# Kernel optimization log

Measured on AMD Instinct MI355X. Metric: run time of the kernel, lower is better.

## Reference

```python
import jax, jax.numpy as jnp
import numpy as np

D = 1024      # input_dim == memory_dim
HID = 1024    # hid_dim
NEG = 1e30


def setup_inputs() -> dict:
    key = jax.random.key(0)
    ks = jax.random.split(key, 9)
    N, LD, LM = 8, 2048, 512
    s = 1.0 / np.sqrt(D)
    return {
        "input": jax.random.normal(ks[0], (N, LD, D), jnp.float32),
        "memory": jax.random.normal(ks[1], (N, LM, D), jnp.float32),
        "mask": jnp.ones((N, LM), jnp.float32),
        # input_linear_1 / memory_linear_1: Linear(d, 1, bias=False)
        "in1_w": jax.random.normal(ks[2], (D,), jnp.float32) * s,
        "mem1_w": jax.random.normal(ks[3], (D,), jnp.float32) * s,
        # input_linear_2 / memory_linear_2: Linear(d, hid, bias=True), stored [d, hid]
        "in2_w": jax.random.normal(ks[4], (D, HID), jnp.float32) * s,
        "in2_b": jax.random.normal(ks[5], (HID,), jnp.float32) * s,
        "mem2_w": jax.random.normal(ks[6], (D, HID), jnp.float32) * s,
        "mem2_b": jax.random.normal(ks[7], (HID,), jnp.float32) * s,
    }


def reference(input, memory, mask, in1_w, mem1_w, in2_w, in2_b, mem2_w, mem2_b):
    # dropout=0.0 / eval mode -> identity
    dot_scale = jnp.asarray(np.sqrt(D), input.dtype)
    input_dot = jnp.einsum("nld,d->nl", input, in1_w)[:, :, None]      # [N,Ld,1]
    memory_dot = jnp.einsum("nmd,d->nm", memory, mem1_w)[:, None, :]   # [N,1,Lm]
    cross_dot = jnp.einsum("nld,nmd->nlm", input, memory) / dot_scale  # [N,Ld,Lm]
    att = input_dot + memory_dot + cross_dot
    att = att - NEG * (1.0 - mask[:, None, :])

    inp2 = jnp.einsum("nld,dh->nlh", input, in2_w) + in2_b    # [N,Ld,hid]
    mem2 = jnp.einsum("nmd,dh->nmh", memory, mem2_w) + mem2_b  # [N,Lm,hid]

    weight_one = jax.nn.softmax(att, axis=-1)                 # [N,Ld,Lm]
    output_one = jnp.einsum("nlm,nmh->nlh", weight_one, mem2)  # [N,Ld,hid]

    weight_two = jax.nn.softmax(jnp.max(att, axis=-1), axis=-1)  # [N,Ld]
    output_two = jnp.einsum("nl,nlh->nh", weight_two, inp2)[:, None, :]  # [N,1,hid]

    out = jnp.concatenate(
        [inp2, output_one, inp2 * output_one, output_two * output_one], axis=-1
    )  # [N,Ld,4*hid]
    return out, mem2
```

## Files before the change

kernel.cpp:

```cpp
#include <hip/hip_runtime.h>

typedef unsigned short u16;
typedef __attribute__((ext_vector_type(8))) short short8;
typedef __attribute__((ext_vector_type(4))) float f32x4;
typedef __attribute__((ext_vector_type(4))) unsigned short u16x4;

#define NSEQ 8
#define LD 2048
#define LM 512
#define DD 1024
#define HID 1024
#define M1 (NSEQ*LD)
#define M2 (NSEQ*LM)

#define GLOAD_LDS16(gp, lp) __builtin_amdgcn_global_load_lds( \
    (const __attribute__((address_space(1))) unsigned int*)(gp), \
    (__attribute__((address_space(3))) unsigned int*)(lp), 16, 0, 0)

__device__ __forceinline__ u16 f2bf(float f) {
    union { float f; unsigned int i; } v; v.f = f;
    unsigned int r = v.i + 0x7fffu + ((v.i >> 16) & 1u);
    return (u16)(r >> 16);
}
__device__ __forceinline__ float bf2f(u16 u) {
    union { unsigned int i; float f; } v; v.i = ((unsigned int)u) << 16; return v.f;
}

__global__ __launch_bounds__(256) void prep_all(
    const float* __restrict__ input, const float* __restrict__ memory,
    const float* __restrict__ in1_w, const float* __restrict__ mem1_w,
    const float* __restrict__ mask,
    const float* __restrict__ in2_w, const float* __restrict__ mem2_w,
    u16* __restrict__ input_bf16, u16* __restrict__ memory_bf16,
    u16* __restrict__ in2_wt, u16* __restrict__ mem2_wt,
    float* __restrict__ idot, float* __restrict__ mdotm) {
    __shared__ float tile[32][33];
    const int b = blockIdx.x, t = threadIdx.x;
    if (b < M1 + M2) {
        const float* src; const float* w; u16* dst;
        if (b < M1) { src = input + (size_t)b * DD; w = in1_w;
                      dst = input_bf16 + (size_t)b * DD; }
        else { const int rm = b - M1; src = memory + (size_t)rm * DD; w = mem1_w;
               dst = memory_bf16 + (size_t)rm * DD; }
        f32x4 v = *(const f32x4*)(src + t * 4);
        f32x4 wv = *(const f32x4*)(w + t * 4);
        u16x4 o;
        #pragma unroll
        for (int i = 0; i < 4; i++) o[i] = f2bf(v[i]);
        *(u16x4*)(dst + t * 4) = o;
        float s = v[0]*wv[0] + v[1]*wv[1] + v[2]*wv[2] + v[3]*wv[3];
        #pragma unroll
        for (int off = 32; off; off >>= 1) s += __shfl_down(s, off);
        if ((t & 63) == 0) tile[0][t >> 6] = s;
        __syncthreads();
        if (t == 0) {
            const float d = tile[0][0] + tile[0][1] + tile[0][2] + tile[0][3];
            if (b < M1) idot[b] = d;
            else { const int rm = b - M1;
                   mdotm[rm] = d - 1e30f * (1.0f - mask[rm]); }
        }
    } else {
        const int wb = b - (M1 + M2);
        const int z = wb >> 10;
        const int tid = wb & 1023;
        const int c0 = (tid & 31) * 32, r0 = (tid >> 5) * 32;
        const float* src = z ? mem2_w : in2_w;
        u16* dst = z ? mem2_wt : in2_wt;
        const int tx = t & 31, ty = t >> 5;
        #pragma unroll
        for (int yy = ty; yy < 32; yy += 8)
            tile[yy][tx] = src[(size_t)(r0 + yy) * DD + c0 + tx];
        __syncthreads();
        #pragma unroll
        for (int yy = ty; yy < 32; yy += 8)
            dst[(size_t)(c0 + yy) * DD + r0 + tx] = f2bf(tile[tx][yy]);
    }
}

template <int NT>
__global__ __launch_bounds__(512, 1) void gemm_mem2(
    const u16* __restrict__ A, const u16* __restrict__ B,
    float* __restrict__ out0, const float* __restrict__ bias,
    u16* __restrict__ mem2t) {
    constexpr int AI = 2, BM = 128;
    constexpr int BUFE = (BM + 128) * 64;
    __shared__ __align__(16) u16 lds[3 * BUFE];
    const int t = threadIdx.x;
    const int lane = t & 63, wave = t >> 6;
    const int wm = wave >> 2, wn = wave & 3;
    const int lr = lane & 15, kg = lane >> 4;
    const int bid = blockIdx.y * 8 + blockIdx.x;
    const int swz = (bid & 7) * gridDim.y + (bid >> 3);
    const int m0 = (swz >> 3) * BM, n0 = (swz & 7) * 128;

    const int srow = lane >> 3;
    const u16* gA[AI];
    const u16* gB[2];
    #pragma unroll
    for (int i = 0; i < AI; i++) {
        const int c = wave * AI + i;
        const int colb = ((lane & 7) * 16) ^ ((((c << 2) + (lane >> 4)) & 7) << 4);
        gA[i] = A + (size_t)(m0 + c * 8 + srow) * DD + (colb >> 1);
    }
    #pragma unroll
    for (int i = 0; i < 2; i++) {
        const int c = wave * 2 + i;
        const int colb = ((lane & 7) * 16) ^ ((((c << 2) + (lane >> 4)) & 7) << 4);
        gB[i] = B + (size_t)(n0 + c * 8 + srow) * DD + (colb >> 1);
    }
    int offA[2 * AI], offB[2];
    #pragma unroll
    for (int i = 0; i < 2 * AI; i++) {
        const int row = wm * (BM / 2) + i * 16 + lr;
        offA[i] = (row * 128 + kg * 16) ^ (((row >> 1) & 7) << 4);
    }
    #pragma unroll
    for (int j = 0; j < 2; j++) {
        const int row = wn * 32 + j * 16 + lr;
        offB[j] = (BM * 64 * 2 + row * 128 + kg * 16) ^ (((row >> 1) & 7) << 4);
    }

    f32x4 acc[2 * AI][2];
    #pragma unroll
    for (int i = 0; i < 2 * AI; i++)
        #pragma unroll
        for (int j = 0; j < 2; j++) acc[i][j] = (f32x4){0.f, 0.f, 0.f, 0.f};

    #define STAGE(tt, buf) do {                                             \
        u16* la_ = &lds[(buf) * BUFE];                                      \
        u16* lb_ = la_ + BM * 64;                                           \
        const int ko_ = (tt) * 64;                                          \
        _Pragma("unroll")                                                   \
        for (int i_ = 0; i_ < AI; i_++)                                     \
            GLOAD_LDS16(gA[i_] + ko_, la_ + (wave * AI + i_) * 512);        \
        _Pragma("unroll")                                                   \
        for (int i_ = 0; i_ < 2; i_++)                                      \
            GLOAD_LDS16(gB[i_] + ko_, lb_ + (wave * 2 + i_) * 512);         \
    } while (0)

    STAGE(0, 0);
    STAGE(1, 1);
    asm volatile("s_waitcnt vmcnt(4)" ::: "memory");
    __builtin_amdgcn_s_barrier();
    __builtin_amdgcn_sched_barrier(0);

    int cb = 0, sb = 2;
    for (int tt = 0; tt < NT; ++tt) {
        if (tt + 2 < NT) STAGE(tt + 2, sb);
        __builtin_amdgcn_sched_barrier(0);
        const char* bb = (const char*)&lds[cb * BUFE];
        short8 bfr[2][2];
        #pragma unroll
        for (int j = 0; j < 2; j++)
            #pragma unroll
            for (int kh = 0; kh < 2; kh++)
                bfr[j][kh] = *(const short8*)(bb + (offB[j] ^ (kh * 64)));
        #pragma unroll
        for (int p = 0; p < AI; p++) {
            short8 af[2][2];
            #pragma unroll
            for (int q = 0; q < 2; q++)
                #pragma unroll
                for (int kh = 0; kh < 2; kh++)
                    af[q][kh] = *(const short8*)(bb + (offA[2 * p + q] ^ (kh * 64)));
            __builtin_amdgcn_s_setprio(1);
            #pragma unroll
            for (int q = 0; q < 2; q++)
                #pragma unroll
                for (int j = 0; j < 2; j++)
                    #pragma unroll
                    for (int kh = 0; kh < 2; kh++)
                        acc[2 * p + q][j] = __builtin_amdgcn_mfma_f32_16x16x32_bf16(
                            af[q][kh], bfr[j][kh], acc[2 * p + q][j], 0, 0, 0);
            __builtin_amdgcn_s_setprio(0);
        }
        if (tt + 2 < NT)      asm volatile("s_waitcnt vmcnt(4)" ::: "memory");
        else if (tt + 1 < NT) asm volatile("s_waitcnt vmcnt(0)" ::: "memory");
        __builtin_amdgcn_s_barrier();
        __builtin_amdgcn_sched_barrier(0);
        cb = (cb == 2) ? 0 : cb + 1;
        sb = (sb == 2) ? 0 : sb + 1;
    }
    #undef STAGE

    u16* ldsT = (u16*)lds;
    #pragma unroll
    for (int i = 0; i < 2 * AI; i++) {
        #pragma unroll
        for (int j = 0; j < 2; j++) {
            const int lcol = wn * 32 + j * 16 + lr;
            const float bv = bias[n0 + lcol];
            #pragma unroll
            for (int r = 0; r < 4; r++) {
                const int lrow = wm * (BM / 2) + i * 16 + kg * 4 + r;
                const float v = acc[i][j][r] + bv;
                out0[(size_t)(m0 + lrow) * HID + n0 + lcol] = v;
                ldsT[lcol * 136 + lrow] = f2bf(v);
            }
        }
    }
    __syncthreads();
    const int nb = m0 >> 9, mloc = m0 & 511;
    #pragma unroll
    for (int s = 0; s < 4; s++) {
        const int idx = s * 512 + t;
        const int hrow = idx >> 4, seg = idx & 15;
        short8 v8 = *(const short8*)&ldsT[hrow * 136 + seg * 8];
        *(short8*)&mem2t[((size_t)nb * HID + n0 + hrow) * LM + mloc + seg * 8] = v8;
    }
}

__global__ __launch_bounds__(512, 2) void fused_gemm(
    const u16* __restrict__ A1, const u16* __restrict__ B1,
    const u16* __restrict__ A2, const u16* __restrict__ B2,
    float* __restrict__ out0,
    const float* __restrict__ bias, const float* __restrict__ ot) {
    constexpr int BUFE = (256 + 128) * 64;
    __shared__ __align__(16) u16 lds[3 * BUFE];
    const int t = threadIdx.x;
    const int lane = t & 63, wave = t >> 6;
    const int wm = wave >> 2, wn = wave & 3;
    const int lr = lane & 15, kg = lane >> 4;
    const int bid = blockIdx.y * 8 + blockIdx.x;
    const int swz = (bid & 7) * gridDim.y + (bid >> 3);
    const int m0 = (swz >> 3) * 256, n0 = (swz & 7) * 128;
    const int nb = m0 / LD;
    const u16* B2p = B2 + (size_t)nb * HID * LM;

    const int srow = lane >> 3;
    int colbA[4], colbB[2];
    const u16* gA[4];
    const u16* gB[2];
    #pragma unroll
    for (int i = 0; i < 4; i++) {
        const int c = wave * 4 + i;
        colbA[i] = ((lane & 7) * 16) ^ ((((c << 2) + (lane >> 4)) & 7) << 4);
        gA[i] = A1 + (size_t)(m0 + c * 8 + srow) * DD + (colbA[i] >> 1);
    }
    #pragma unroll
    for (int i = 0; i < 2; i++) {
        const int c = wave * 2 + i;
        colbB[i] = ((lane & 7) * 16) ^ ((((c << 2) + (lane >> 4)) & 7) << 4);
        gB[i] = B1 + (size_t)(n0 + c * 8 + srow) * DD + (colbB[i] >> 1);
    }
    int offA[8], offB[2];
    #pragma unroll
    for (int i = 0; i < 8; i++) {
        const int row = wm * 128 + i * 16 + lr;
        offA[i] = (row * 128 + kg * 16) ^ (((row >> 1) & 7) << 4);
    }
    #pragma unroll
    for (int j = 0; j < 2; j++) {
        const int row = wn * 32 + j * 16 + lr;
        offB[j] = (256 * 64 * 2 + row * 128 + kg * 16) ^ (((row >> 1) & 7) << 4);
    }

    #define STAGE(tt, buf) do {                                             \
        u16* la_ = &lds[(buf) * BUFE];                                      \
        u16* lb_ = la_ + 256 * 64;                                          \
        const int ko_ = (tt) * 64;                                          \
        _Pragma("unroll")                                                   \
        for (int i_ = 0; i_ < 4; i_++)                                      \
            GLOAD_LDS16(gA[i_] + ko_, la_ + (wave * 4 + i_) * 512);         \
        _Pragma("unroll")                                                   \
        for (int i_ = 0; i_ < 2; i_++)                                      \
            GLOAD_LDS16(gB[i_] + ko_, lb_ + (wave * 2 + i_) * 512);         \
    } while (0)

    #define KLOOP(NT, ACC)                                                  \
    do {                                                                    \
        STAGE(0, 0);                                                        \
        STAGE(1, 1);                                                        \
        asm volatile("s_waitcnt vmcnt(6)" ::: "memory");                    \
        __builtin_amdgcn_s_barrier();                                       \
        __builtin_amdgcn_sched_barrier(0);                                  \
        int cb = 0, sb = 2;                                                 \
        for (int tt = 0; tt < (NT); ++tt) {                                 \
            if (tt + 2 < (NT)) STAGE(tt + 2, sb);                           \
            __builtin_amdgcn_sched_barrier(0);                              \
            const char* bb = (const char*)&lds[cb * BUFE];                  \
            short8 bfr[2][2];                                               \
            _Pragma("unroll")                                               \
            for (int j = 0; j < 2; j++)                                     \
                _Pragma("unroll")                                           \
                for (int kh = 0; kh < 2; kh++)                              \
                    bfr[j][kh] = *(const short8*)(bb + (offB[j] ^ (kh * 64))); \
            _Pragma("unroll")                                               \
            for (int p = 0; p < 4; p++) {                                   \
                short8 af[2][2];                                            \
                _Pragma("unroll")                                           \
                for (int q = 0; q < 2; q++)                                 \
                    _Pragma("unroll")                                       \
                    for (int kh = 0; kh < 2; kh++)                          \
                        af[q][kh] = *(const short8*)(bb + (offA[2 * p + q] ^ (kh * 64))); \
                __builtin_amdgcn_s_setprio(1);                              \
                _Pragma("unroll")                                           \
                for (int q = 0; q < 2; q++)                                 \
                    _Pragma("unroll")                                       \
                    for (int j = 0; j < 2; j++)                             \
                        _Pragma("unroll")                                   \
                        for (int kh = 0; kh < 2; kh++)                      \
                            ACC[2 * p + q][j] = __builtin_amdgcn_mfma_f32_16x16x32_bf16( \
                                af[q][kh], bfr[j][kh], ACC[2 * p + q][j], 0, 0, 0); \
                __builtin_amdgcn_s_setprio(0);                              \
            }                                                               \
            if (tt + 2 < (NT))      asm volatile("s_waitcnt vmcnt(6)" ::: "memory"); \
            else if (tt + 1 < (NT)) asm volatile("s_waitcnt vmcnt(0)" ::: "memory"); \
            __builtin_amdgcn_s_barrier();                                   \
            __builtin_amdgcn_sched_barrier(0);                              \
            cb = (cb == 2) ? 0 : cb + 1;                                    \
            sb = (sb == 2) ? 0 : sb + 1;                                    \
        }                                                                   \
    } while (0)

    f32x4 acc1[8][2], acc2[8][2];
    #pragma unroll
    for (int i = 0; i < 8; i++)
        #pragma unroll
        for (int j = 0; j < 2; j++) {
            acc1[i][j] = (f32x4){0.f, 0.f, 0.f, 0.f};
            acc2[i][j] = (f32x4){0.f, 0.f, 0.f, 0.f};
        }

    KLOOP(16, acc1);

    #pragma unroll
    for (int i = 0; i < 4; i++) {
        const int c = wave * 4 + i;
        gA[i] = A2 + (size_t)(m0 + c * 8 + srow) * LM + (colbA[i] >> 1);
    }
    #pragma unroll
    for (int i = 0; i < 2; i++) {
        const int c = wave * 2 + i;
        gB[i] = B2p + (size_t)(n0 + c * 8 + srow) * LM + (colbB[i] >> 1);
    }

    KLOOP(8, acc2);

    #undef KLOOP
    #undef STAGE

    #pragma unroll
    for (int i = 0; i < 8; i++) {
        #pragma unroll
        for (int j = 0; j < 2; j++) {
            const int col = n0 + wn * 32 + j * 16 + lr;
            const float b = bias[col];
            const float otv = ot[nb * HID + col];
            #pragma unroll
            for (int r = 0; r < 4; r++) {
                const int row = m0 + wm * 128 + i * 16 + kg * 4 + r;
                const size_t o = (size_t)row * 4096 + col;
                const float i2 = acc1[i][j][r] + b;
                const float o1 = acc2[i][j][r];
                out0[o] = i2;
                out0[o + 1024] = o1;
                out0[o + 2048] = i2 * o1;
                out0[o + 3072] = otv * o1;
            }
        }
    }
}

__global__ __launch_bounds__(512, 1) void att_softmax(
    const u16* __restrict__ A, const u16* __restrict__ B,
    const float* __restrict__ idot, const float* __restrict__ mdotm,
    u16* __restrict__ P, float* __restrict__ rowmax) {
    constexpr int ABUF = 64 * 64;
    constexpr int BBUF = 256 * 64;
    constexpr int BUFE = ABUF + BBUF;
    __shared__ __align__(16) u16 lds[3 * BUFE];
    const int t = threadIdx.x, lane = t & 63, wave = t >> 6;
    const int wm = wave >> 2, wn = wave & 3;
    const int lr = lane & 15, kg = lane >> 4;
    const int bid = blockIdx.x;
    const int swz = (bid & 7) * 32 + (bid >> 3);
    const int m0 = swz * 64;
    const int nb = m0 >> 11;
    const u16* Bp = B + (size_t)nb * LM * DD;

    const int srow = lane >> 3;
    const u16* gA;
    {
        const int colb = ((lane & 7) * 16) ^ ((((wave << 2) + (lane >> 4)) & 7) << 4);
        gA = A + (size_t)(m0 + wave * 8 + srow) * DD + (colb >> 1);
    }
    const u16* gB[4];
    #pragma unroll
    for (int i = 0; i < 4; i++) {
        const int c = wave * 4 + i;
        const int colb = ((lane & 7) * 16) ^ ((((c << 2) + (lane >> 4)) & 7) << 4);
        gB[i] = Bp + (size_t)(c * 8 + srow) * DD + (colb >> 1);
    }
    int offA[2], offB[4];
    #pragma unroll
    for (int i = 0; i < 2; i++) {
        const int row = wm * 32 + i * 16 + lr;
        offA[i] = (row * 128 + kg * 16) ^ (((row >> 1) & 7) << 4);
    }
    #pragma unroll
    for (int j = 0; j < 4; j++) {
        const int row = wn * 64 + j * 16 + lr;
        offB[j] = (ABUF * 2 + row * 128 + kg * 16) ^ (((row >> 1) & 7) << 4);
    }

    f32x4 acc[2][8];
    #pragma unroll
    for (int i = 0; i < 2; i++)
        #pragma unroll
        for (int j = 0; j < 8; j++) acc[i][j] = (f32x4){0.f, 0.f, 0.f, 0.f};

    #define ASTAGE(tt, buf, pofs) do {                                      \
        u16* la_ = &lds[(buf) * BUFE];                                      \
        u16* lb_ = la_ + ABUF;                                              \
        const int ko_ = (tt) * 64;                                          \
        GLOAD_LDS16(gA + ko_, la_ + wave * 512);                            \
        _Pragma("unroll")                                                   \
        for (int i_ = 0; i_ < 4; i_++)                                      \
            GLOAD_LDS16(gB[i_] + (pofs) + ko_, lb_ + (wave * 4 + i_) * 512); \
    } while (0)

    for (int c = 0; c < 2; c++) {
        const size_t pofs = (size_t)c * 256 * DD;
        ASTAGE(0, 0, pofs);
        ASTAGE(1, 1, pofs);
        asm volatile("s_waitcnt vmcnt(5)" ::: "memory");
        __builtin_amdgcn_s_barrier();
        __builtin_amdgcn_sched_barrier(0);
        int cb = 0, sb = 2;
        for (int tt = 0; tt < 16; ++tt) {
            if (tt + 2 < 16) ASTAGE(tt + 2, sb, pofs);
            __builtin_amdgcn_sched_barrier(0);
            const char* bb = (const char*)&lds[cb * BUFE];
            short8 af[2][2];
            #pragma unroll
            for (int i = 0; i < 2; i++)
                #pragma unroll
                for (int kh = 0; kh < 2; kh++)
                    af[i][kh] = *(const short8*)(bb + (offA[i] ^ (kh * 64)));
            #pragma unroll
            for (int j = 0; j < 4; j++) {
                short8 bf[2];
                #pragma unroll
                for (int kh = 0; kh < 2; kh++)
                    bf[kh] = *(const short8*)(bb + (offB[j] ^ (kh * 64)));
                __builtin_amdgcn_s_setprio(1);
                #pragma unroll
                for (int i = 0; i < 2; i++)
                    #pragma unroll
                    for (int kh = 0; kh < 2; kh++)
                        acc[i][c * 4 + j] = __builtin_amdgcn_mfma_f32_16x16x32_bf16(
                            af[i][kh], bf[kh], acc[i][c * 4 + j], 0, 0, 0);
                __builtin_amdgcn_s_setprio(0);
            }
            if (tt + 2 < 16)      asm volatile("s_waitcnt vmcnt(5)" ::: "memory");
            else if (tt + 1 < 16) asm volatile("s_waitcnt vmcnt(0)" ::: "memory");
            __builtin_amdgcn_s_barrier();
            __builtin_amdgcn_sched_barrier(0);
            cb = (cb == 2) ? 0 : cb + 1;
            sb = (sb == 2) ? 0 : sb + 1;
        }
    }
    #undef ASTAGE

    float* redm = (float*)lds;
    float* reds = redm + 256;
    float mdv[8];
    #pragma unroll
    for (int cj = 0; cj < 8; cj++)
        mdv[cj] = mdotm[nb * LM + (cj >> 2) * 256 + wn * 64 + (cj & 3) * 16 + lr];
    float idv[8];
    #pragma unroll
    for (int i = 0; i < 2; i++)
        #pragma unroll
        for (int r = 0; r < 4; r++)
            idv[i * 4 + r] = idot[m0 + wm * 32 + i * 16 + kg * 4 + r];
    float pm[8];
    #pragma unroll
    for (int i = 0; i < 2; i++)
        #pragma unroll
        for (int r = 0; r < 4; r++) {
            float mx = -3.0e38f;
            #pragma unroll
            for (int cj = 0; cj < 8; cj++) {
                const float v = acc[i][cj][r] * 0.03125f + idv[i * 4 + r] + mdv[cj];
                acc[i][cj][r] = v;
                mx = fmaxf(mx, v);
            }
            pm[i * 4 + r] = mx;
        }
    #pragma unroll
    for (int w = 1; w < 16; w <<= 1)
        #pragma unroll
        for (int q = 0; q < 8; q++) pm[q] = fmaxf(pm[q], __shfl_xor(pm[q], w));
    if (lr == 0) {
        #pragma unroll
        for (int i = 0; i < 2; i++)
            #pragma unroll
            for (int r = 0; r < 4; r++)
                redm[(wm * 32 + i * 16 + kg * 4 + r) * 4 + wn] = pm[i * 4 + r];
    }
    __syncthreads();
    float Mr[8], ps[8];
    #pragma unroll
    for (int i = 0; i < 2; i++)
        #pragma unroll
        for (int r = 0; r < 4; r++) {
            const int row = wm * 32 + i * 16 + kg * 4 + r;
            const float a = fmaxf(redm[row * 4 + 0], redm[row * 4 + 1]);
            const float b = fmaxf(redm[row * 4 + 2], redm[row * 4 + 3]);
            Mr[i * 4 + r] = fmaxf(a, b);
            float s = 0.f;
            #pragma unroll
            for (int cj = 0; cj < 8; cj++) {
                const float e = __expf(acc[i][cj][r] - Mr[i * 4 + r]);
                acc[i][cj][r] = e;
                s += e;
            }
            ps[i * 4 + r] = s;
        }
    #pragma unroll
    for (int w = 1; w < 16; w <<= 1)
        #pragma unroll
        for (int q = 0; q < 8; q++) ps[q] += __shfl_xor(ps[q], w);
    if (lr == 0) {
        #pragma unroll
        for (int i = 0; i < 2; i++)
            #pragma unroll
            for (int r = 0; r < 4; r++)
                reds[(wm * 32 + i * 16 + kg * 4 + r) * 4 + wn] = ps[i * 4 + r];
    }
    __syncthreads();
    #pragma unroll
    for (int i = 0; i < 2; i++)
        #pragma unroll
        for (int r = 0; r < 4; r++) {
            const int row = wm * 32 + i * 16 + kg * 4 + r;
            const float inv = 1.0f / (reds[row * 4 + 0] + reds[row * 4 + 1] +
                                      reds[row * 4 + 2] + reds[row * 4 + 3]);
            if (wn == 0 && lr == 0) rowmax[m0 + row] = Mr[i * 4 + r];
            #pragma unroll
            for (int cj = 0; cj < 8; cj++)
                P[(size_t)(m0 + row) * LM +
                  (cj >> 2) * 256 + wn * 64 + (cj & 3) * 16 + lr] =
                    f2bf(acc[i][cj][r] * inv);
        }
}

__global__ __launch_bounds__(256) void xbar_partial(
    const float* __restrict__ rowmax, const u16* __restrict__ X,
    float* __restrict__ part) {
    const int lz = blockIdx.x, n = blockIdx.y, t = threadIdx.x;
    const float* rm = rowmax + (size_t)n * LD;
    float v[8];
    float m = -3.0e38f;
    #pragma unroll
    for (int i = 0; i < 8; i++) { v[i] = rm[t + i * 256]; m = fmaxf(m, v[i]); }
    #pragma unroll
    for (int off = 32; off; off >>= 1) m = fmaxf(m, __shfl_down(m, off));
    __shared__ float sm[4], ss[4];
    __shared__ float wl[64];
    if ((t & 63) == 0) sm[t >> 6] = m;
    __syncthreads();
    const float M = fmaxf(fmaxf(sm[0], sm[1]), fmaxf(sm[2], sm[3]));
    float s = 0.f;
    #pragma unroll
    for (int i = 0; i < 8; i++) s += __expf(v[i] - M);
    #pragma unroll
    for (int off = 32; off; off >>= 1) s += __shfl_down(s, off);
    if ((t & 63) == 0) ss[t >> 6] = s;
    __syncthreads();
    const float invS = 1.0f / (ss[0] + ss[1] + ss[2] + ss[3]);
    if (t < 64) wl[t] = __expf(rm[lz * 64 + t] - M) * invS;
    __syncthreads();
    const u16* xp = X + ((size_t)n * LD + lz * 64) * DD + t * 4;
    f32x4 acc = {0.f, 0.f, 0.f, 0.f};
    #pragma unroll 4
    for (int l = 0; l < 64; l++) {
        u16x4 x = *(const u16x4*)(xp + (size_t)l * DD);
        const float w = wl[l];
        acc[0] += w * bf2f(x[0]); acc[1] += w * bf2f(x[1]);
        acc[2] += w * bf2f(x[2]); acc[3] += w * bf2f(x[3]);
    }
    *(f32x4*)&part[((size_t)n * 32 + lz) * HID + t * 4] = acc;
}

__global__ __launch_bounds__(256) void ot_final2(
    const float* __restrict__ part, const u16* __restrict__ Wt,
    const float* __restrict__ bias, float* __restrict__ ot) {
    const int hc = blockIdx.x, n = blockIdx.y, t = threadIdx.x;
    __shared__ float xb[HID];
    f32x4 s = {0.f, 0.f, 0.f, 0.f};
    #pragma unroll
    for (int i = 0; i < 32; i++) {
        f32x4 p = *(const f32x4*)&part[((size_t)n * 32 + i) * HID + t * 4];
        s[0] += p[0]; s[1] += p[1]; s[2] += p[2]; s[3] += p[3];
    }
    *(f32x4*)&xb[t * 4] = s;
    __syncthreads();
    const int h = hc * 128 + (t >> 1);
    const int d0 = (t & 1) * 512;
    float a = 0.f;
    #pragma unroll 4
    for (int d = 0; d < 512; d += 8) {
        short8 w8 = *(const short8*)&Wt[(size_t)h * DD + d0 + d];
        #pragma unroll
        for (int j = 0; j < 8; j++) a += bf2f((u16)w8[j]) * xb[d0 + d + j];
    }
    a += __shfl_xor(a, 1);
    if ((t & 1) == 0) ot[(size_t)n * HID + h] = a + bias[h];
}

extern "C" void kernel_launch(void* const* d_in, const int* in_sizes, int n_in,
                              void* d_out, int out_size, void* d_ws, size_t ws_size,
                              hipStream_t stream) {
    const float* input  = (const float*)d_in[0];
    const float* memory = (const float*)d_in[1];
    const float* mask   = (const float*)d_in[2];
    const float* in1_w  = (const float*)d_in[3];
    const float* mem1_w = (const float*)d_in[4];
    const float* in2_w  = (const float*)d_in[5];
    const float* in2_b  = (const float*)d_in[6];
    const float* mem2_w = (const float*)d_in[7];
    const float* mem2_b = (const float*)d_in[8];

    float* out = (float*)d_out;
    float* outTail = out + (size_t)M1 * 4096;

    char* ws = (char*)d_ws;
    size_t off = 0;
    auto alloc = [&](size_t bytes) -> void* {
        void* p = ws + off;
        off = (off + bytes + 255) & ~(size_t)255;
        return p;
    };
    u16* input_bf16  = (u16*)alloc((size_t)M1 * DD * 2);
    u16* memory_bf16 = (u16*)alloc((size_t)M2 * DD * 2);
    u16* in2_wt      = (u16*)alloc((size_t)HID * DD * 2);
    u16* mem2_wt     = (u16*)alloc((size_t)HID * DD * 2);
    u16* mem2t       = (u16*)alloc((size_t)NSEQ * HID * LM * 2);
    u16* P           = (u16*)alloc((size_t)M1 * LM * 2);
    float* idot      = (float*)alloc((size_t)M1 * 4);
    float* mdotm     = (float*)alloc((size_t)M2 * 4);
    float* rowmax    = (float*)alloc((size_t)M1 * 4);
    float* ot        = (float*)alloc((size_t)NSEQ * HID * 4);
    float* part      = (float*)alloc((size_t)NSEQ * 32 * HID * 4);

    prep_all<<<M1 + M2 + 2048, 256, 0, stream>>>(
        input, memory, in1_w, mem1_w, mask, in2_w, mem2_w,
        input_bf16, memory_bf16, in2_wt, mem2_wt, idot, mdotm);
    gemm_mem2<16><<<dim3(8, M2 / 128), 512, 0, stream>>>(
        memory_bf16, mem2_wt, outTail, mem2_b, mem2t);
    att_softmax<<<M1 / 64, 512, 0, stream>>>(
        input_bf16, memory_bf16, idot, mdotm, P, rowmax);
    xbar_partial<<<dim3(32, NSEQ), 256, 0, stream>>>(rowmax, input_bf16, part);
    ot_final2<<<dim3(8, NSEQ), 256, 0, stream>>>(part, in2_wt, in2_b, ot);
    fused_gemm<<<dim3(8, M1 / 256), 512, 0, stream>>>(
        input_bf16, in2_wt, P, mem2t, out, in2_b, ot);
}
```

Baseline: 196.8 us.

## Merge mem2 GEMM and attention softmax into one launch; shrink fused_gemm tile

Combines the mem2 projection GEMM and the attention-score/softmax kernel into one kernel, with block index deciding which role each block takes. Both halves get 256 blocks each on one grid. This removes a kernel launch and lets the two independent workloads fill the GPU together instead of each underfilling it. Separately, fused_gemm moves from 256-row tiles with 2 blocks/CU to 128-row tiles with 1 block/CU, doubling its grid, which trades per-block reuse for more parallelism.

```diff
diff --git a/kernel.cpp b/kernel.cpp
--- a/kernel.cpp
+++ b/kernel.cpp
@@ -77,11 +77,322 @@
     }
 }
 
-template <int NT>
-__global__ __launch_bounds__(512, 1) void gemm_mem2(
+__global__ __launch_bounds__(512, 1) void mm_att(
     const u16* __restrict__ A, const u16* __restrict__ B,
-    float* __restrict__ out0, const float* __restrict__ bias,
-    u16* __restrict__ mem2t) {
+    const float* __restrict__ idot, const float* __restrict__ mdotm,
+    u16* __restrict__ P, float* __restrict__ rowmax,
+    const u16* __restrict__ Wm, float* __restrict__ out0,
+    const float* __restrict__ bias, u16* __restrict__ mem2t) {
+    __shared__ __align__(16) u16 lds[61440];
+    const int t = threadIdx.x, lane = t & 63, wave = t >> 6;
+    const int wm = wave >> 2, wn = wave & 3;
+    const int lr = lane & 15, kg = lane >> 4;
+    const int srow = lane >> 3;
+
+    if (blockIdx.x < 256) {
+        constexpr int ABUF = 64 * 64;
+        constexpr int BBUF = 256 * 64;
+        constexpr int BUFE = ABUF + BBUF;
+        const int bid = blockIdx.x;
+        const int swz = (bid & 7) * 32 + (bid >> 3);
+        const int m0 = swz * 64;
+        const int nb = m0 >> 11;
+        const u16* Bp = B + (size_t)nb * LM * DD;
+
+        const u16* gA;
+        {
+            const int colb = ((lane & 7) * 16) ^ ((((wave << 2) + (lane >> 4)) & 7) << 4);
+            gA = A + (size_t)(m0 + wave * 8 + srow) * DD + (colb >> 1);
+        }
+        const u16* gB[4];
+        #pragma unroll
+        for (int i = 0; i < 4; i++) {
+            const int c = wave * 4 + i;
+            const int colb = ((lane & 7) * 16) ^ ((((c << 2) + (lane >> 4)) & 7) << 4);
+            gB[i] = Bp + (size_t)(c * 8 + srow) * DD + (colb >> 1);
+        }
+        int offA[2], offB[4];
+        #pragma unroll
+        for (int i = 0; i < 2; i++) {
+            const int row = wm * 32 + i * 16 + lr;
+            offA[i] = (row * 128 + kg * 16) ^ (((row >> 1) & 7) << 4);
+        }
+        #pragma unroll
+        for (int j = 0; j < 4; j++) {
+            const int row = wn * 64 + j * 16 + lr;
+            offB[j] = (ABUF * 2 + row * 128 + kg * 16) ^ (((row >> 1) & 7) << 4);
+        }
+
+        f32x4 acc[2][8];
+        #pragma unroll
+        for (int i = 0; i < 2; i++)
+            #pragma unroll
+            for (int j = 0; j < 8; j++) acc[i][j] = (f32x4){0.f, 0.f, 0.f, 0.f};
+
+        #define ASTAGE(tt, buf, pofs) do {                                  \
+            u16* la_ = &lds[(buf) * BUFE];                                  \
+            u16* lb_ = la_ + ABUF;                                          \
+            const int ko_ = (tt) * 64;                                      \
+            GLOAD_LDS16(gA + ko_, la_ + wave * 512);                        \
+            _Pragma("unroll")                                               \
+            for (int i_ = 0; i_ < 4; i_++)                                  \
+                GLOAD_LDS16(gB[i_] + (pofs) + ko_, lb_ + (wave * 4 + i_) * 512); \
+        } while (0)
+
+        for (int c = 0; c < 2; c++) {
+            const size_t pofs = (size_t)c * 256 * DD;
+            ASTAGE(0, 0, pofs);
+            ASTAGE(1, 1, pofs);
+            asm volatile("s_waitcnt vmcnt(5)" ::: "memory");
+            __builtin_amdgcn_s_barrier();
+            __builtin_amdgcn_sched_barrier(0);
+            int cb = 0, sb = 2;
+            for (int tt = 0; tt < 16; ++tt) {
+                if (tt + 2 < 16) ASTAGE(tt + 2, sb, pofs);
+                __builtin_amdgcn_sched_barrier(0);
+                const char* bb = (const char*)&lds[cb * BUFE];
+                short8 af[2][2];
+                #pragma unroll
+                for (int i = 0; i < 2; i++)
+                    #pragma unroll
+                    for (int kh = 0; kh < 2; kh++)
+                        af[i][kh] = *(const short8*)(bb + (offA[i] ^ (kh * 64)));
+                #pragma unroll
+                for (int j = 0; j < 4; j++) {
+                    short8 bf[2];
+                    #pragma unroll
+                    for (int kh = 0; kh < 2; kh++)
+                        bf[kh] = *(const short8*)(bb + (offB[j] ^ (kh * 64)));
+                    __builtin_amdgcn_s_setprio(1);
+                    #pragma unroll
+                    for (int i = 0; i < 2; i++)
+                        #pragma unroll
+                        for (int kh = 0; kh < 2; kh++)
+                            acc[i][c * 4 + j] = __builtin_amdgcn_mfma_f32_16x16x32_bf16(
+                                af[i][kh], bf[kh], acc[i][c * 4 + j], 0, 0, 0);
+                    __builtin_amdgcn_s_setprio(0);
+                }
+                if (tt + 2 < 16)      asm volatile("s_waitcnt vmcnt(5)" ::: "memory");
+                else if (tt + 1 < 16) asm volatile("s_waitcnt vmcnt(0)" ::: "memory");
+                __builtin_amdgcn_s_barrier();
+                __builtin_amdgcn_sched_barrier(0);
+                cb = (cb == 2) ? 0 : cb + 1;
+                sb = (sb == 2) ? 0 : sb + 1;
+            }
+        }
+        #undef ASTAGE
+
+        float* redm = (float*)lds;
+        float* reds = redm + 256;
+        float mdv[8];
+        #pragma unroll
+        for (int cj = 0; cj < 8; cj++)
+            mdv[cj] = mdotm[nb * LM + (cj >> 2) * 256 + wn * 64 + (cj & 3) * 16 + lr];
+        float idv[8];
+        #pragma unroll
+        for (int i = 0; i < 2; i++)
+            #pragma unroll
+            for (int r = 0; r < 4; r++)
+                idv[i * 4 + r] = idot[m0 + wm * 32 + i * 16 + kg * 4 + r];
+        float pm[8];
+        #pragma unroll
+        for (int i = 0; i < 2; i++)
+            #pragma unroll
+            for (int r = 0; r < 4; r++) {
+                float mx = -3.0e38f;
+                #pragma unroll
+                for (int cj = 0; cj < 8; cj++) {
+                    const float v = acc[i][cj][r] * 0.03125f + idv[i * 4 + r] + mdv[cj];
+                    acc[i][cj][r] = v;
+                    mx = fmaxf(mx, v);
+                }
+                pm[i * 4 + r] = mx;
+            }
+        #pragma unroll
+        for (int w = 1; w < 16; w <<= 1)
+            #pragma unroll
+            for (int q = 0; q < 8; q++) pm[q] = fmaxf(pm[q], __shfl_xor(pm[q], w));
+        if (lr == 0) {
+            #pragma unroll
+            for (int i = 0; i < 2; i++)
+                #pragma unroll
+                for (int r = 0; r < 4; r++)
+                    redm[(wm * 32 + i * 16 + kg * 4 + r) * 4 + wn] = pm[i * 4 + r];
+        }
+        __syncthreads();
+        float Mr[8], ps[8];
+        #pragma unroll
+        for (int i = 0; i < 2; i++)
+            #pragma unroll
+            for (int r = 0; r < 4; r++) {
+                const int row = wm * 32 + i * 16 + kg * 4 + r;
+                const float a = fmaxf(redm[row * 4 + 0], redm[row * 4 + 1]);
+                const float b2 = fmaxf(redm[row * 4 + 2], redm[row * 4 + 3]);
+                Mr[i * 4 + r] = fmaxf(a, b2);
+                float s = 0.f;
+                #pragma unroll
+                for (int cj = 0; cj < 8; cj++) {
+                    const float e = __expf(acc[i][cj][r] - Mr[i * 4 + r]);
+                    acc[i][cj][r] = e;
+                    s += e;
+                }
+                ps[i * 4 + r] = s;
+            }
+        #pragma unroll
+        for (int w = 1; w < 16; w <<= 1)
+            #pragma unroll
+            for (int q = 0; q < 8; q++) ps[q] += __shfl_xor(ps[q], w);
+        if (lr == 0) {
+            #pragma unroll
+            for (int i = 0; i < 2; i++)
+                #pragma unroll
+                for (int r = 0; r < 4; r++)
+                    reds[(wm * 32 + i * 16 + kg * 4 + r) * 4 + wn] = ps[i * 4 + r];
+        }
+        __syncthreads();
+        #pragma unroll
+        for (int i = 0; i < 2; i++)
+            #pragma unroll
+            for (int r = 0; r < 4; r++) {
+                const int row = wm * 32 + i * 16 + kg * 4 + r;
+                const float inv = 1.0f / (reds[row * 4 + 0] + reds[row * 4 + 1] +
+                                          reds[row * 4 + 2] + reds[row * 4 + 3]);
+                if (wn == 0 && lr == 0) rowmax[m0 + row] = Mr[i * 4 + r];
+                #pragma unroll
+                for (int cj = 0; cj < 8; cj++)
+                    P[(size_t)(m0 + row) * LM +
+                      (cj >> 2) * 256 + wn * 64 + (cj & 3) * 16 + lr] =
+                        f2bf(acc[i][cj][r] * inv);
+            }
+    } else {
+        constexpr int AI = 2, BM = 128;
+        constexpr int BUFE = (BM + 128) * 64;
+        const int bid = blockIdx.x - 256;
+        const int swz = (bid & 7) * 32 + (bid >> 3);
+        const int m0 = (swz >> 3) * BM, n0 = (swz & 7) * 128;
+
+        const u16* gA[AI];
+        const u16* gB[2];
+        #pragma unroll
+        for (int i = 0; i < AI; i++) {
+            const int c = wave * AI + i;
+            const int colb = ((lane & 7) * 16) ^ ((((c << 2) + (lane >> 4)) & 7) << 4);
+            gA[i] = B  + (size_t)(m0 + c * 8 + srow) * DD + (colb >> 1);
+        }
+        #pragma unroll
+        for (int i = 0; i < 2; i++) {
+            const int c = wave * 2 + i;
+            const int colb = ((lane & 7) * 16) ^ ((((c << 2) + (lane >> 4)) & 7) << 4);
+            gB[i] = Wm + (size_t)(n0 + c * 8 + srow) * DD + (colb >> 1);
+        }
+        int offA[2 * AI], offB[2];
+        #pragma unroll
+        for (int i = 0; i < 2 * AI; i++) {
+            const int row = wm * (BM / 2) + i * 16 + lr;
+            offA[i] = (row * 128 + kg * 16) ^ (((row >> 1) & 7) << 4);
+        }
+        #pragma unroll
+        for (int j = 0; j < 2; j++) {
+            const int row = wn * 32 + j * 16 + lr;
+            offB[j] = (BM * 64 * 2 + row * 128 + kg * 16) ^ (((row >> 1) & 7) << 4);
+        }
+
+        f32x4 acc[2 * AI][2];
+        #pragma unroll
+        for (int i = 0; i < 2 * AI; i++)
+            #pragma unroll
+            for (int j = 0; j < 2; j++) acc[i][j] = (f32x4){0.f, 0.f, 0.f, 0.f};
+
+        #define MSTAGE(tt, buf) do {                                        \
+            u16* la_ = &lds[(buf) * BUFE];                                  \
+            u16* lb_ = la_ + BM * 64;                                       \
+            const int ko_ = (tt) * 64;                                      \
+            _Pragma("unroll")                                               \
+            for (int i_ = 0; i_ < AI; i_++)                                 \
+                GLOAD_LDS16(gA[i_] + ko_, la_ + (wave * AI + i_) * 512);    \
+            _Pragma("unroll")                                               \
+            for (int i_ = 0; i_ < 2; i_++)                                  \
+                GLOAD_LDS16(gB[i_] + ko_, lb_ + (wave * 2 + i_) * 512);     \
+        } while (0)
+
+        MSTAGE(0, 0);
+        MSTAGE(1, 1);
+        asm volatile("s_waitcnt vmcnt(4)" ::: "memory");
+        __builtin_amdgcn_s_barrier();
+        __builtin_amdgcn_sched_barrier(0);
+
+        int cb = 0, sb = 2;
+        for (int tt = 0; tt < 16; ++tt) {
+            if (tt + 2 < 16) MSTAGE(tt + 2, sb);
+            __builtin_amdgcn_sched_barrier(0);
+            const char* bb = (const char*)&lds[cb * BUFE];
+            short8 bfr[2][2];
+            #pragma unroll
+            for (int j = 0; j < 2; j++)
+                #pragma unroll
+                for (int kh = 0; kh < 2; kh++)
+                    bfr[j][kh] = *(const short8*)(bb + (offB[j] ^ (kh * 64)));
+            #pragma unroll
+            for (int p = 0; p < AI; p++) {
+                short8 af[2][2];
+                #pragma unroll
+                for (int q = 0; q < 2; q++)
+                    #pragma unroll
+                    for (int kh = 0; kh < 2; kh++)
+                        af[q][kh] = *(const short8*)(bb + (offA[2 * p + q] ^ (kh * 64)));
+                __builtin_amdgcn_s_setprio(1);
+                #pragma unroll
+                for (int q = 0; q < 2; q++)
+                    #pragma unroll
+                    for (int j = 0; j < 2; j++)
+                        #pragma unroll
+                        for (int kh = 0; kh < 2; kh++)
+                            acc[2 * p + q][j] = __builtin_amdgcn_mfma_f32_16x16x32_bf16(
+                                af[q][kh], bfr[j][kh], acc[2 * p + q][j], 0, 0, 0);
+                __builtin_amdgcn_s_setprio(0);
+            }
+            if (tt + 2 < 16)      asm volatile("s_waitcnt vmcnt(4)" ::: "memory");
+            else if (tt + 1 < 16) asm volatile("s_waitcnt vmcnt(0)" ::: "memory");
+            __builtin_amdgcn_s_barrier();
+            __builtin_amdgcn_sched_barrier(0);
+            cb = (cb == 2) ? 0 : cb + 1;
+            sb = (sb == 2) ? 0 : sb + 1;
+        }
+        #undef MSTAGE
+
+        u16* ldsT = (u16*)lds;
+        #pragma unroll
+        for (int i = 0; i < 2 * AI; i++) {
+            #pragma unroll
+            for (int j = 0; j < 2; j++) {
+                const int lcol = wn * 32 + j * 16 + lr;
+                const float bv = bias[n0 + lcol];
+                #pragma unroll
+                for (int r = 0; r < 4; r++) {
+                    const int lrow = wm * (BM / 2) + i * 16 + kg * 4 + r;
+                    const float v = acc[i][j][r] + bv;
+                    out0[(size_t)(m0 + lrow) * HID + n0 + lcol] = v;
+                    ldsT[lcol * 136 + lrow] = f2bf(v);
+                }
+            }
+        }
+        __syncthreads();
+        const int nb = m0 >> 9, mloc = m0 & 511;
+        #pragma unroll
+        for (int s = 0; s < 4; s++) {
+            const int idx = s * 512 + t;
+            const int hrow = idx >> 4, seg = idx & 15;
+            short8 v8 = *(const short8*)&ldsT[hrow * 136 + seg * 8];
+            *(short8*)&mem2t[((size_t)nb * HID + n0 + hrow) * LM + mloc + seg * 8] = v8;
+        }
+    }
+}
+
+__global__ __launch_bounds__(512, 1) void fused_gemm(
+    const u16* __restrict__ A1, const u16* __restrict__ B1,
+    const u16* __restrict__ A2, const u16* __restrict__ B2,
+    float* __restrict__ out0,
+    const float* __restrict__ bias, const float* __restrict__ ot) {
     constexpr int AI = 2, BM = 128;
     constexpr int BUFE = (BM + 128) * 64;
     __shared__ __align__(16) u16 lds[3 * BUFE];
@@ -92,21 +403,24 @@
     const int bid = blockIdx.y * 8 + blockIdx.x;
     const int swz = (bid & 7) * gridDim.y + (bid >> 3);
     const int m0 = (swz >> 3) * BM, n0 = (swz & 7) * 128;
+    const int nb = m0 / LD;
+    const u16* B2p = B2 + (size_t)nb * HID * LM;
 
     const int srow = lane >> 3;
+    int colbA[AI], colbB[2];
     const u16* gA[AI];
     const u16* gB[2];
     #pragma unroll
     for (int i = 0; i < AI; i++) {
         const int c = wave * AI + i;
-        const int colb = ((lane & 7) * 16) ^ ((((c << 2) + (lane >> 4)) & 7) << 4);
-        gA[i] = A + (size_t)(m0 + c * 8 + srow) * DD + (colb >> 1);
+        colbA[i] = ((lane & 7) * 16) ^ ((((c << 2) + (lane >> 4)) & 7) << 4);
+        gA[i] = A1 + (size_t)(m0 + c * 8 + srow) * DD + (colbA[i] >> 1);
     }
     #pragma unroll
     for (int i = 0; i < 2; i++) {
         const int c = wave * 2 + i;
-        const int colb = ((lane & 7) * 16) ^ ((((c << 2) + (lane >> 4)) & 7) << 4);
-        gB[i] = B + (size_t)(n0 + c * 8 + srow) * DD + (colb >> 1);
+        colbB[i] = ((lane & 7) * 16) ^ ((((c << 2) + (lane >> 4)) & 7) << 4);
+        gB[i] = B1 + (size_t)(n0 + c * 8 + srow) * DD + (colbB[i] >> 1);
     }
     int offA[2 * AI], offB[2];
     #pragma unroll
@@ -119,12 +433,6 @@
         const int row = wn * 32 + j * 16 + lr;
         offB[j] = (BM * 64 * 2 + row * 128 + kg * 16) ^ (((row >> 1) & 7) << 4);
     }
-
-    f32x4 acc[2 * AI][2];
-    #pragma unroll
-    for (int i = 0; i < 2 * AI; i++)
-        #pragma unroll
-        for (int j = 0; j < 2; j++) acc[i][j] = (f32x4){0.f, 0.f, 0.f, 0.f};
 
     #define STAGE(tt, buf) do {                                             \
         u16* la_ = &lds[(buf) * BUFE];                                      \
@@ -138,140 +446,11 @@
             GLOAD_LDS16(gB[i_] + ko_, lb_ + (wave * 2 + i_) * 512);         \
     } while (0)
 
-    STAGE(0, 0);
-    STAGE(1, 1);
-    asm volatile("s_waitcnt vmcnt(4)" ::: "memory");
-    __builtin_amdgcn_s_barrier();
-    __builtin_amdgcn_sched_barrier(0);
-
-    int cb = 0, sb = 2;
-    for (int tt = 0; tt < NT; ++tt) {
-        if (tt + 2 < NT) STAGE(tt + 2, sb);
-        __builtin_amdgcn_sched_barrier(0);
-        const char* bb = (const char*)&lds[cb * BUFE];
-        short8 bfr[2][2];
-        #pragma unroll
-        for (int j = 0; j < 2; j++)
-            #pragma unroll
-            for (int kh = 0; kh < 2; kh++)
-                bfr[j][kh] = *(const short8*)(bb + (offB[j] ^ (kh * 64)));
-        #pragma unroll
-        for (int p = 0; p < AI; p++) {
-            short8 af[2][2];
-            #pragma unroll
-            for (int q = 0; q < 2; q++)
-                #pragma unroll
-                for (int kh = 0; kh < 2; kh++)
-                    af[q][kh] = *(const short8*)(bb + (offA[2 * p + q] ^ (kh * 64)));
-            __builtin_amdgcn_s_setprio(1);
-            #pragma unroll
-            for (int q = 0; q < 2; q++)
-                #pragma unroll
-                for (int j = 0; j < 2; j++)
-                    #pragma unroll
-                    for (int kh = 0; kh < 2; kh++)
-                        acc[2 * p + q][j] = __builtin_amdgcn_mfma_f32_16x16x32_bf16(
-                            af[q][kh], bfr[j][kh], acc[2 * p + q][j], 0, 0, 0);
-            __builtin_amdgcn_s_setprio(0);
-        }
-        if (tt + 2 < NT)      asm volatile("s_waitcnt vmcnt(4)" ::: "memory");
-        else if (tt + 1 < NT) asm volatile("s_waitcnt vmcnt(0)" ::: "memory");
-        __builtin_amdgcn_s_barrier();
-        __builtin_amdgcn_sched_barrier(0);
-        cb = (cb == 2) ? 0 : cb + 1;
-        sb = (sb == 2) ? 0 : sb + 1;
-    }
-    #undef STAGE
-
-    u16* ldsT = (u16*)lds;
-    #pragma unroll
-    for (int i = 0; i < 2 * AI; i++) {
-        #pragma unroll
-        for (int j = 0; j < 2; j++) {
-            const int lcol = wn * 32 + j * 16 + lr;
-            const float bv = bias[n0 + lcol];
-            #pragma unroll
-            for (int r = 0; r < 4; r++) {
-                const int lrow = wm * (BM / 2) + i * 16 + kg * 4 + r;
-                const float v = acc[i][j][r] + bv;
-                out0[(size_t)(m0 + lrow) * HID + n0 + lcol] = v;
-                ldsT[lcol * 136 + lrow] = f2bf(v);
-            }
-        }
-    }
-    __syncthreads();
-    const int nb = m0 >> 9, mloc = m0 & 511;
-    #pragma unroll
-    for (int s = 0; s < 4; s++) {
-        const int idx = s * 512 + t;
-        const int hrow = idx >> 4, seg = idx & 15;
-        short8 v8 = *(const short8*)&ldsT[hrow * 136 + seg * 8];
-        *(short8*)&mem2t[((size_t)nb * HID + n0 + hrow) * LM + mloc + seg * 8] = v8;
-    }
-}
-
-__global__ __launch_bounds__(512, 2) void fused_gemm(
-    const u16* __restrict__ A1, const u16* __restrict__ B1,
-    const u16* __restrict__ A2, const u16* __restrict__ B2,
-    float* __restrict__ out0,
-    const float* __restrict__ bias, const float* __restrict__ ot) {
-    constexpr int BUFE = (256 + 128) * 64;
-    __shared__ __align__(16) u16 lds[3 * BUFE];
-    const int t = threadIdx.x;
-    const int lane = t & 63, wave = t >> 6;
-    const int wm = wave >> 2, wn = wave & 3;
-    const int lr = lane & 15, kg = lane >> 4;
-    const int bid = blockIdx.y * 8 + blockIdx.x;
-    const int swz = (bid & 7) * gridDim.y + (bid >> 3);
-    const int m0 = (swz >> 3) * 256, n0 = (swz & 7) * 128;
-    const int nb = m0 / LD;
-    const u16* B2p = B2 + (size_t)nb * HID * LM;
-
-    const int srow = lane >> 3;
-    int colbA[4], colbB[2];
-    const u16* gA[4];
-    const u16* gB[2];
-    #pragma unroll
-    for (int i = 0; i < 4; i++) {
-        const int c = wave * 4 + i;
-        colbA[i] = ((lane & 7) * 16) ^ ((((c << 2) + (lane >> 4)) & 7) << 4);
-        gA[i] = A1 + (size_t)(m0 + c * 8 + srow) * DD + (colbA[i] >> 1);
-    }
-    #pragma unroll
-    for (int i = 0; i < 2; i++) {
-        const int c = wave * 2 + i;
-        colbB[i] = ((lane & 7) * 16) ^ ((((c << 2) + (lane >> 4)) & 7) << 4);
-        gB[i] = B1 + (size_t)(n0 + c * 8 + srow) * DD + (colbB[i] >> 1);
-    }
-    int offA[8], offB[2];
-    #pragma unroll
-    for (int i = 0; i < 8; i++) {
-        const int row = wm * 128 + i * 16 + lr;
-        offA[i] = (row * 128 + kg * 16) ^ (((row >> 1) & 7) << 4);
-    }
-    #pragma unroll
-    for (int j = 0; j < 2; j++) {
-        const int row = wn * 32 + j * 16 + lr;
-        offB[j] = (256 * 64 * 2 + row * 128 + kg * 16) ^ (((row >> 1) & 7) << 4);
-    }
-
-    #define STAGE(tt, buf) do {                                             \
-        u16* la_ = &lds[(buf) * BUFE];                                      \
-        u16* lb_ = la_ + 256 * 64;                                          \
-        const int ko_ = (tt) * 64;                                          \
-        _Pragma("unroll")                                                   \
-        for (int i_ = 0; i_ < 4; i_++)                                      \
-            GLOAD_LDS16(gA[i_] + ko_, la_ + (wave * 4 + i_) * 512);         \
-        _Pragma("unroll")                                                   \
-        for (int i_ = 0; i_ < 2; i_++)                                      \
-            GLOAD_LDS16(gB[i_] + ko_, lb_ + (wave * 2 + i_) * 512);         \
-    } while (0)
-
     #define KLOOP(NT, ACC)                                                  \
     do {                                                                    \
         STAGE(0, 0);                                                        \
         STAGE(1, 1);                                                        \
-        asm volatile("s_waitcnt vmcnt(6)" ::: "memory");                    \
+        asm volatile("s_waitcnt vmcnt(4)" ::: "memory");                    \
         __builtin_amdgcn_s_barrier();                                       \
         __builtin_amdgcn_sched_barrier(0);                                  \
         int cb = 0, sb = 2;                                                 \
@@ -286,7 +465,7 @@
                 for (int kh = 0; kh < 2; kh++)                              \
                     bfr[j][kh] = *(const short8*)(bb + (offB[j] ^ (kh * 64))); \
             _Pragma("unroll")                                               \
-            for (int p = 0; p < 4; p++) {                                   \
+            for (int p = 0; p < AI; p++) {                                  \
                 short8 af[2][2];                                            \
                 _Pragma("unroll")                                           \
                 for (int q = 0; q < 2; q++)                                 \
@@ -304,7 +483,7 @@
                                 af[q][kh], bfr[j][kh], ACC[2 * p + q][j], 0, 0, 0); \
                 __builtin_amdgcn_s_setprio(0);                              \
             }                                                               \
-            if (tt + 2 < (NT))      asm volatile("s_waitcnt vmcnt(6)" ::: "memory"); \
+            if (tt + 2 < (NT))      asm volatile("s_waitcnt vmcnt(4)" ::: "memory"); \
             else if (tt + 1 < (NT)) asm volatile("s_waitcnt vmcnt(0)" ::: "memory"); \
             __builtin_amdgcn_s_barrier();                                   \
             __builtin_amdgcn_sched_barrier(0);                              \
@@ -313,9 +492,9 @@
         }                                                                   \
     } while (0)
 
-    f32x4 acc1[8][2], acc2[8][2];
-    #pragma unroll
-    for (int i = 0; i < 8; i++)
+    f32x4 acc1[2 * AI][2], acc2[2 * AI][2];
+    #pragma unroll
+    for (int i = 0; i < 2 * AI; i++)
         #pragma unroll
         for (int j = 0; j < 2; j++) {
             acc1[i][j] = (f32x4){0.f, 0.f, 0.f, 0.f};
@@ -325,8 +504,8 @@
     KLOOP(16, acc1);
 
     #pragma unroll
-    for (int i = 0; i < 4; i++) {
-        const int c = wave * 4 + i;
+    for (int i = 0; i < AI; i++) {
+        const int c = wave * AI + i;
         gA[i] = A2 + (size_t)(m0 + c * 8 + srow) * LM + (colbA[i] >> 1);
     }
     #pragma unroll
@@ -341,7 +520,7 @@
     #undef STAGE
 
     #pragma unroll
-    for (int i = 0; i < 8; i++) {
+    for (int i = 0; i < 2 * AI; i++) {
         #pragma unroll
         for (int j = 0; j < 2; j++) {
             const int col = n0 + wn * 32 + j * 16 + lr;
@@ -349,7 +528,7 @@
             const float otv = ot[nb * HID + col];
             #pragma unroll
             for (int r = 0; r < 4; r++) {
-                const int row = m0 + wm * 128 + i * 16 + kg * 4 + r;
+                const int row = m0 + wm * (BM / 2) + i * 16 + kg * 4 + r;
                 const size_t o = (size_t)row * 4096 + col;
                 const float i2 = acc1[i][j][r] + b;
                 const float o1 = acc2[i][j][r];
@@ -360,191 +539,6 @@
             }
         }
     }
-}
-
-__global__ __launch_bounds__(512, 1) void att_softmax(
-    const u16* __restrict__ A, const u16* __restrict__ B,
-    const float* __restrict__ idot, const float* __restrict__ mdotm,
-    u16* __restrict__ P, float* __restrict__ rowmax) {
-    constexpr int ABUF = 64 * 64;
-    constexpr int BBUF = 256 * 64;
-    constexpr int BUFE = ABUF + BBUF;
-    __shared__ __align__(16) u16 lds[3 * BUFE];
-    const int t = threadIdx.x, lane = t & 63, wave = t >> 6;
-    const int wm = wave >> 2, wn = wave & 3;
-    const int lr = lane & 15, kg = lane >> 4;
-    const int bid = blockIdx.x;
-    const int swz = (bid & 7) * 32 + (bid >> 3);
-    const int m0 = swz * 64;
-    const int nb = m0 >> 11;
-    const u16* Bp = B + (size_t)nb * LM * DD;
-
-    const int srow = lane >> 3;
-    const u16* gA;
-    {
-        const int colb = ((lane & 7) * 16) ^ ((((wave << 2) + (lane >> 4)) & 7) << 4);
-        gA = A + (size_t)(m0 + wave * 8 + srow) * DD + (colb >> 1);
-    }
-    const u16* gB[4];
-    #pragma unroll
-    for (int i = 0; i < 4; i++) {
-        const int c = wave * 4 + i;
-        const int colb = ((lane & 7) * 16) ^ ((((c << 2) + (lane >> 4)) & 7) << 4);
-        gB[i] = Bp + (size_t)(c * 8 + srow) * DD + (colb >> 1);
-    }
-    int offA[2], offB[4];
-    #pragma unroll
-    for (int i = 0; i < 2; i++) {
-        const int row = wm * 32 + i * 16 + lr;
-        offA[i] = (row * 128 + kg * 16) ^ (((row >> 1) & 7) << 4);
-    }
-    #pragma unroll
-    for (int j = 0; j < 4; j++) {
-        const int row = wn * 64 + j * 16 + lr;
-        offB[j] = (ABUF * 2 + row * 128 + kg * 16) ^ (((row >> 1) & 7) << 4);
-    }
-
-    f32x4 acc[2][8];
-    #pragma unroll
-    for (int i = 0; i < 2; i++)
-        #pragma unroll
-        for (int j = 0; j < 8; j++) acc[i][j] = (f32x4){0.f, 0.f, 0.f, 0.f};
-
-    #define ASTAGE(tt, buf, pofs) do {                                      \
-        u16* la_ = &lds[(buf) * BUFE];                                      \
-        u16* lb_ = la_ + ABUF;                                              \
-        const int ko_ = (tt) * 64;                                          \
-        GLOAD_LDS16(gA + ko_, la_ + wave * 512);                            \
-        _Pragma("unroll")                                                   \
-        for (int i_ = 0; i_ < 4; i_++)                                      \
-            GLOAD_LDS16(gB[i_] + (pofs) + ko_, lb_ + (wave * 4 + i_) * 512); \
-    } while (0)
-
-    for (int c = 0; c < 2; c++) {
-        const size_t pofs = (size_t)c * 256 * DD;
-        ASTAGE(0, 0, pofs);
-        ASTAGE(1, 1, pofs);
-        asm volatile("s_waitcnt vmcnt(5)" ::: "memory");
-        __builtin_amdgcn_s_barrier();
-        __builtin_amdgcn_sched_barrier(0);
-        int cb = 0, sb = 2;
-        for (int tt = 0; tt < 16; ++tt) {
-            if (tt + 2 < 16) ASTAGE(tt + 2, sb, pofs);
-            __builtin_amdgcn_sched_barrier(0);
-            const char* bb = (const char*)&lds[cb * BUFE];
-            short8 af[2][2];
-            #pragma unroll
-            for (int i = 0; i < 2; i++)
-                #pragma unroll
-                for (int kh = 0; kh < 2; kh++)
-                    af[i][kh] = *(const short8*)(bb + (offA[i] ^ (kh * 64)));
-            #pragma unroll
-            for (int j = 0; j < 4; j++) {
-                short8 bf[2];
-                #pragma unroll
-                for (int kh = 0; kh < 2; kh++)
-                    bf[kh] = *(const short8*)(bb + (offB[j] ^ (kh * 64)));
-                __builtin_amdgcn_s_setprio(1);
-                #pragma unroll
-                for (int i = 0; i < 2; i++)
-                    #pragma unroll
-                    for (int kh = 0; kh < 2; kh++)
-                        acc[i][c * 4 + j] = __builtin_amdgcn_mfma_f32_16x16x32_bf16(
-                            af[i][kh], bf[kh], acc[i][c * 4 + j], 0, 0, 0);
-                __builtin_amdgcn_s_setprio(0);
-            }
-            if (tt + 2 < 16)      asm volatile("s_waitcnt vmcnt(5)" ::: "memory");
-            else if (tt + 1 < 16) asm volatile("s_waitcnt vmcnt(0)" ::: "memory");
-            __builtin_amdgcn_s_barrier();
-            __builtin_amdgcn_sched_barrier(0);
-            cb = (cb == 2) ? 0 : cb + 1;
-            sb = (sb == 2) ? 0 : sb + 1;
-        }
-    }
-    #undef ASTAGE
-
-    float* redm = (float*)lds;
-    float* reds = redm + 256;
-    float mdv[8];
-    #pragma unroll
-    for (int cj = 0; cj < 8; cj++)
-        mdv[cj] = mdotm[nb * LM + (cj >> 2) * 256 + wn * 64 + (cj & 3) * 16 + lr];
-    float idv[8];
-    #pragma unroll
-    for (int i = 0; i < 2; i++)
-        #pragma unroll
-        for (int r = 0; r < 4; r++)
-            idv[i * 4 + r] = idot[m0 + wm * 32 + i * 16 + kg * 4 + r];
-    float pm[8];
-    #pragma unroll
-    for (int i = 0; i < 2; i++)
-        #pragma unroll
-        for (int r = 0; r < 4; r++) {
-            float mx = -3.0e38f;
-            #pragma unroll
-            for (int cj = 0; cj < 8; cj++) {
-                const float v = acc[i][cj][r] * 0.03125f + idv[i * 4 + r] + mdv[cj];
-                acc[i][cj][r] = v;
-                mx = fmaxf(mx, v);
-            }
-            pm[i * 4 + r] = mx;
-        }
-    #pragma unroll
-    for (int w = 1; w < 16; w <<= 1)
-        #pragma unroll
-        for (int q = 0; q < 8; q++) pm[q] = fmaxf(pm[q], __shfl_xor(pm[q], w));
-    if (lr == 0) {
-        #pragma unroll
-        for (int i = 0; i < 2; i++)
-            #pragma unroll
-            for (int r = 0; r < 4; r++)
-                redm[(wm * 32 + i * 16 + kg * 4 + r) * 4 + wn] = pm[i * 4 + r];
-    }
-    __syncthreads();
-    float Mr[8], ps[8];
-    #pragma unroll
-    for (int i = 0; i < 2; i++)
-        #pragma unroll
-        for (int r = 0; r < 4; r++) {
-            const int row = wm * 32 + i * 16 + kg * 4 + r;
-            const float a = fmaxf(redm[row * 4 + 0], redm[row * 4 + 1]);
-            const float b = fmaxf(redm[row * 4 + 2], redm[row * 4 + 3]);
-            Mr[i * 4 + r] = fmaxf(a, b);
-            float s = 0.f;
-            #pragma unroll
-            for (int cj = 0; cj < 8; cj++) {
-                const float e = __expf(acc[i][cj][r] - Mr[i * 4 + r]);
-                acc[i][cj][r] = e;
-                s += e;
-            }
-            ps[i * 4 + r] = s;
-        }
-    #pragma unroll
-    for (int w = 1; w < 16; w <<= 1)
-        #pragma unroll
-        for (int q = 0; q < 8; q++) ps[q] += __shfl_xor(ps[q], w);
-    if (lr == 0) {
-        #pragma unroll
-        for (int i = 0; i < 2; i++)
-            #pragma unroll
-            for (int r = 0; r < 4; r++)
-                reds[(wm * 32 + i * 16 + kg * 4 + r) * 4 + wn] = ps[i * 4 + r];
-    }
-    __syncthreads();
-    #pragma unroll
-    for (int i = 0; i < 2; i++)
-        #pragma unroll
-        for (int r = 0; r < 4; r++) {
-            const int row = wm * 32 + i * 16 + kg * 4 + r;
-            const float inv = 1.0f / (reds[row * 4 + 0] + reds[row * 4 + 1] +
-                                      reds[row * 4 + 2] + reds[row * 4 + 3]);
-            if (wn == 0 && lr == 0) rowmax[m0 + row] = Mr[i * 4 + r];
-            #pragma unroll
-            for (int cj = 0; cj < 8; cj++)
-                P[(size_t)(m0 + row) * LM +
-                  (cj >> 2) * 256 + wn * 64 + (cj & 3) * 16 + lr] =
-                    f2bf(acc[i][cj][r] * inv);
-        }
 }
 
 __global__ __launch_bounds__(256) void xbar_partial(
@@ -649,12 +643,11 @@
     prep_all<<<M1 + M2 + 2048, 256, 0, stream>>>(
         input, memory, in1_w, mem1_w, mask, in2_w, mem2_w,
         input_bf16, memory_bf16, in2_wt, mem2_wt, idot, mdotm);
-    gemm_mem2<16><<<dim3(8, M2 / 128), 512, 0, stream>>>(
-        memory_bf16, mem2_wt, outTail, mem2_b, mem2t);
-    att_softmax<<<M1 / 64, 512, 0, stream>>>(
-        input_bf16, memory_bf16, idot, mdotm, P, rowmax);
+    mm_att<<<512, 512, 0, stream>>>(
+        input_bf16, memory_bf16, idot, mdotm, P, rowmax,
+        mem2_wt, outTail, mem2_b, mem2t);
     xbar_partial<<<dim3(32, NSEQ), 256, 0, stream>>>(rowmax, input_bf16, part);
     ot_final2<<<dim3(8, NSEQ), 256, 0, stream>>>(part, in2_wt, in2_b, ot);
-    fused_gemm<<<dim3(8, M1 / 256), 512, 0, stream>>>(
+    fused_gemm<<<dim3(8, M1 / 128), 512, 0, stream>>>(
         input_bf16, in2_wt, P, mem2t, out, in2_b, ot);
 }
```

New measurement: 199.4 us. No clear change (+1.3%).
